# Kernel tuning notes

Hardware: AMD Instinct MI355X
Metric: run time of the kernel (lower is better)

Reference implementation:

```python
import jax, jax.numpy as jnp
import numpy as np

B, S, D, H = 4, 2048, 1024, 16
DH = D // H  # dim per head

def setup_inputs() -> dict:
    key = jax.random.key(0)
    ks = jax.random.split(key, 12)
    sc = 1.0 / np.sqrt(D)
    inp = {
        "key": jax.random.normal(ks[0], (B, S, D), jnp.float32),
        "value": jax.random.normal(ks[1], (B, S, D), jnp.float32),
        "query": jax.random.normal(ks[2], (B, S, D), jnp.float32),
        "mask": jax.random.randint(ks[3], (B, S, S), 0, 2).astype(bool),
        "Wq": jax.random.normal(ks[4], (D, D), jnp.float32) * sc,
        "bq": jnp.zeros((D,), jnp.float32),
        "Wk": jax.random.normal(ks[5], (D, D), jnp.float32) * sc,
        "bk": jnp.zeros((D,), jnp.float32),
        "Wv": jax.random.normal(ks[6], (D, D), jnp.float32) * sc,
        "bv": jnp.zeros((D,), jnp.float32),
        "Wo": jax.random.normal(ks[7], (D, D), jnp.float32) * sc,
        "bo": jnp.zeros((D,), jnp.float32),
    }
    return inp

def _shape(x, b):
    # [b, len, D] -> [b, H, len, DH]
    return x.reshape(b, -1, H, DH).transpose(0, 2, 1, 3)

def reference(key, value, query, mask, Wq, bq, Wk, bk, Wv, bv, Wo, bo):
    b = key.shape[0]
    q = _shape(query @ Wq.T + bq, b) / jnp.sqrt(jnp.asarray(DH, query.dtype))
    k = _shape(key @ Wk.T + bk, b)
    v = _shape(value @ Wv.T + bv, b)
    # scores: [b, H, q_len, k_len]
    scores = jnp.einsum("bhqd,bhkd->bhqk", q, k)
    scores = jnp.where(mask[:, None, :, :], jnp.asarray(-1e18, scores.dtype), scores)
    attn = jax.nn.softmax(scores, axis=-1)  # dropout is identity in eval mode
    ctx = jnp.einsum("bhqk,bhkd->bhqd", attn, v)
    ctx = ctx.transpose(0, 2, 1, 3).reshape(b, -1, H * DH)
    return ctx @ Wo.T + bo
```

## Files before the change

kernel.cpp:

```cpp
#include <hip/hip_runtime.h>

#define BB  4
#define SS  2048
#define DD  1024
#define HH  16
#define DHH 64
#define LOG2E 1.44269504088896340736f

typedef __attribute__((ext_vector_type(8)))  _Float16 half8;
typedef __attribute__((ext_vector_type(4)))  _Float16 half4;
typedef __attribute__((ext_vector_type(2)))  float    f32x2;
typedef __attribute__((ext_vector_type(4)))  float    f32x4;
typedef __attribute__((ext_vector_type(8)))  float    f32x8;
typedef __attribute__((ext_vector_type(16))) float    f32x16;
typedef __attribute__((ext_vector_type(4)))  unsigned int uint4v;

#if __has_builtin(__builtin_amdgcn_exp2f)
#define EXP2(x) __builtin_amdgcn_exp2f(x)
#else
#define EXP2(x) exp2f(x)
#endif

#if __has_builtin(__builtin_amdgcn_sbfe)
#define SBIT(x, p) __builtin_amdgcn_sbfe((int)(x), (unsigned)(p), 1u)
#else
#define SBIT(x, p) (((int)((x) << (31 - (p)))) >> 31)
#endif

__device__ __forceinline__ void gload_lds16(const void* g, void* l) {
  __builtin_amdgcn_global_load_lds(
      (const __attribute__((address_space(1))) unsigned int*)g,
      (__attribute__((address_space(3))) unsigned int*)l, 16, 0, 0);
}

__device__ __forceinline__ void plswap(unsigned int& x, unsigned int& y) {
  auto r = __builtin_amdgcn_permlane32_swap(x, y, false, false);
  x = r[0]; y = r[1];
}
__device__ __forceinline__ float xhalf_sum(float v) {
  unsigned int x = __builtin_bit_cast(unsigned int, v), y = x;
  plswap(x, y);
  return __builtin_bit_cast(float, x) + __builtin_bit_cast(float, y);
}

__device__ __forceinline__ float tree8(f32x8 u) {
  f32x4 v = __builtin_shufflevector(u, u, 0, 1, 2, 3) +
            __builtin_shufflevector(u, u, 4, 5, 6, 7);
  f32x2 w2 = __builtin_shufflevector(v, v, 0, 1) + __builtin_shufflevector(v, v, 2, 3);
  return w2[0] + w2[1];
}

__global__ __launch_bounds__(256) void cvt_f32_f16(
    const float* __restrict__ in, _Float16* __restrict__ out, int n4) {
  int i = blockIdx.x * 256 + threadIdx.x;
  if (i >= n4) return;
  float4 a = reinterpret_cast<const float4*>(in)[i];
  half4 h;
  h[0] = (_Float16)a.x; h[1] = (_Float16)a.y;
  h[2] = (_Float16)a.z; h[3] = (_Float16)a.w;
  reinterpret_cast<half4*>(out)[i] = h;
}

__global__ __launch_bounds__(256) void cvt_in3(
    const float* __restrict__ s0, const float* __restrict__ s1,
    const float* __restrict__ s2,
    _Float16* __restrict__ d0, _Float16* __restrict__ d1,
    _Float16* __restrict__ d2, int n4) {
  int i = blockIdx.x * 256 + threadIdx.x;
  if (i >= n4) return;
  const float* s; _Float16* d;
  switch (blockIdx.y) {
    case 0: s = s0; d = d0; break;
    case 1: s = s1; d = d1; break;
    default: s = s2; d = d2; break;
  }
  float4 a = reinterpret_cast<const float4*>(s)[i];
  half4 h;
  h[0] = (_Float16)a.x; h[1] = (_Float16)a.y;
  h[2] = (_Float16)a.z; h[3] = (_Float16)a.w;
  reinterpret_cast<half4*>(d)[i] = h;
}

__global__ __launch_bounds__(256) void cvt_w4(
    const float* __restrict__ s0, const float* __restrict__ s1,
    const float* __restrict__ s2, const float* __restrict__ s3,
    _Float16* __restrict__ d0, _Float16* __restrict__ d1,
    _Float16* __restrict__ d2, _Float16* __restrict__ d3, int n4) {
  int i = blockIdx.x * 256 + threadIdx.x;
  if (i >= n4) return;
  const float* s; _Float16* d;
  switch (blockIdx.y) {
    case 0: s = s0; d = d0; break;
    case 1: s = s1; d = d1; break;
    case 2: s = s2; d = d2; break;
    default: s = s3; d = d3; break;
  }
  float4 a = reinterpret_cast<const float4*>(s)[i];
  half4 h;
  h[0] = (_Float16)a.x; h[1] = (_Float16)a.y;
  h[2] = (_Float16)a.z; h[3] = (_Float16)a.w;
  reinterpret_cast<half4*>(d)[i] = h;
}

__global__ __launch_bounds__(256) void pack_mask_kernel(
    const int* __restrict__ m, unsigned long long* __restrict__ bitsT) {
  size_t g = (size_t)blockIdx.x * 256 + threadIdx.x;
  unsigned long long bal = __ballot(m[g] != 0);
  if ((threadIdx.x & 63) == 0) {
    int key = (int)(g & (SS - 1));
    int q   = (int)((g >> 11) & (SS - 1));
    int b   = (int)(g >> 22);
    bitsT[((size_t)(b * (SS / 64) + (key >> 6))) * SS + q] = bal;
  }
}


#define GEMM_BODY(A, Bm, K)                                                       \
  __shared__ _Float16 lsA[128 * 64];                                              \
  __shared__ _Float16 lsB[128 * 64];                                              \
  const int t = threadIdx.x;                                                      \
  const int w = t >> 6, l = t & 63;                                               \
  const int l15 = l & 15, l4 = l >> 4;                                            \
  const int wm = (w >> 1) * 64, wn = (w & 1) * 64;                                \
  const int srow = l >> 3;                                                        \
  const int scolh = ((l & 7) ^ srow) * 8;                                         \
  f32x4 acc[4][4] = {};                                                           \
  const _Float16* gA = (A) + (size_t)(tm * 128) * (K);                            \
  const _Float16* gB = (Bm) + (size_t)(tn * 128) * (K);                           \
  for (int kt = 0; kt < (K); kt += 64) {                                          \
    _Pragma("unroll") for (int i = 0; i < 4; ++i) {                               \
      int c = w * 4 + i;                                                          \
      int row = c * 8 + srow;                                                     \
      gload_lds16(gA + (size_t)row * (K) + kt + scolh, lsA + c * 512);            \
      gload_lds16(gB + (size_t)row * (K) + kt + scolh, lsB + c * 512);            \
    }                                                                             \
    __syncthreads();                                                              \
    _Pragma("unroll") for (int kk = 0; kk < 2; ++kk) {                            \
      half8 aF[4], bF[4];                                                         \
      _Pragma("unroll") for (int x = 0; x < 4; ++x) {                             \
        int ra = wm + x * 16 + l15;                                               \
        aF[x] = *(const half8*)(lsA + ra * 64 + ((kk * 32 + l4 * 8) ^ ((ra & 7) * 8))); \
        int rb = wn + x * 16 + l15;                                               \
        bF[x] = *(const half8*)(lsB + rb * 64 + ((kk * 32 + l4 * 8) ^ ((rb & 7) * 8))); \
      }                                                                           \
      _Pragma("unroll") for (int x = 0; x < 4; ++x)                               \
        _Pragma("unroll") for (int y = 0; y < 4; ++y)                             \
          acc[x][y] = __builtin_amdgcn_mfma_f32_16x16x32_f16(aF[x], bF[y], acc[x][y], 0, 0, 0); \
    }                                                                             \
    __syncthreads();                                                              \
  }

template <int MODE>
__global__ __launch_bounds__(256, 3) void gemm_nt(
    const _Float16* __restrict__ A, const _Float16* __restrict__ Bm,
    const float* __restrict__ bias, void* __restrict__ out,
    int M, int N, int K, int tilesN) {
  const int nb8 = gridDim.x >> 3;
  const int bidx = (blockIdx.x & 7) * nb8 + (blockIdx.x >> 3);
  const int tm = bidx / tilesN, tn = bidx % tilesN;
  GEMM_BODY(A, Bm, K)
#pragma unroll
  for (int x = 0; x < 4; ++x) {
#pragma unroll
    for (int r = 0; r < 4; ++r) {
      int i = tm * 128 + wm + x * 16 + l4 * 4 + r;
#pragma unroll
      for (int y = 0; y < 4; ++y) {
        int j = tn * 128 + wn + y * 16 + l15;
        float v = acc[x][y][r];
        if (MODE == 0) {
          v = (v + bias[j]) * (0.125f * LOG2E);
          ((_Float16*)out)[(((size_t)(i >> 11) * HH + (j >> 6)) * SS + (i & (SS - 1))) * DHH + (j & 63)] =
              (_Float16)v;
        } else if (MODE == 1) {
          v = v + bias[j];
          ((_Float16*)out)[(((size_t)(i >> 11) * HH + (j >> 6)) * SS + (i & (SS - 1))) * DHH + (j & 63)] =
              (_Float16)v;
        } else if (MODE == 2) {
          v = v + bias[i];
          ((_Float16*)out)[((size_t)(j >> 11) * DD + i) * SS + (j & (SS - 1))] = (_Float16)v;
        } else {
          ((float*)out)[(size_t)i * N + j] = v + bias[j];
        }
      }
    }
  }
}

__global__ __launch_bounds__(256, 3) void gemm_qk(
    const _Float16* __restrict__ xq, const _Float16* __restrict__ xk,
    const _Float16* __restrict__ wq, const _Float16* __restrict__ wk,
    const float* __restrict__ bq, const float* __restrict__ bk,
    _Float16* __restrict__ qh, _Float16* __restrict__ kh) {
  const int bidx = (blockIdx.x & 7) * 128 + (blockIdx.x >> 3);
  const int half = bidx >> 9;
  const int hb = bidx & 511;
  const int tm = hb >> 3, tn = hb & 7;
  const _Float16* A  = half ? xk : xq;
  const _Float16* Bm = half ? wk : wq;
  const float* bias  = half ? bk : bq;
  _Float16* dst      = half ? kh : qh;
  const float scl    = half ? 1.0f : (0.125f * LOG2E);
  GEMM_BODY(A, Bm, DD)
#pragma unroll
  for (int x = 0; x < 4; ++x) {
#pragma unroll
    for (int r = 0; r < 4; ++r) {
      int i = tm * 128 + wm + x * 16 + l4 * 4 + r;
#pragma unroll
      for (int y = 0; y < 4; ++y) {
        int j = tn * 128 + wn + y * 16 + l15;
        float v = (acc[x][y][r] + bias[j]) * scl;
        dst[(((size_t)(i >> 11) * HH + (j >> 6)) * SS + (i & (SS - 1))) * DHH + (j & 63)] =
            (_Float16)v;
      }
    }
  }
}

__global__ __launch_bounds__(256, 4) void attn_kernel(
    const _Float16* __restrict__ qh, const _Float16* __restrict__ kh,
    const _Float16* __restrict__ vt, const unsigned long long* __restrict__ mT,
    _Float16* __restrict__ ctx) {
  __shared__ _Float16 lsK[2][64 * 64];
  __shared__ _Float16 lsV[2][64 * 64];

  const int t = threadIdx.x;
  const int w = t >> 6, l = t & 63;
  const int l31 = l & 31, hi = l >> 5;
  const int srow = l >> 3;
  const int scolh = ((l & 7) ^ srow) * 8;

  const int bid = ((blockIdx.x & 7) << 7) | (blockIdx.x >> 3);
  const int bh = bid >> 4;
  const int qt = bid & 15;
  const int b = bh >> 4;
  const int h = bh & 15;
  const int qbase = qt * 128 + w * 32;

  const _Float16* qrow = qh + ((size_t)bh * SS + qbase + l31) * DHH + hi * 8;
  half8 bQ[4];
#pragma unroll
  for (int s = 0; s < 4; ++s) bQ[s] = *(const half8*)(qrow + s * 16);

  const _Float16* kbh = kh + (size_t)bh * SS * DHH;
  const _Float16* vbh = vt + (size_t)bh * DHH * SS;

  int boff[2][4];
  {
    const int swzb = (l31 & 7) * 16;
#pragma unroll
    for (int i = 0; i < 2; ++i)
#pragma unroll
      for (int s = 0; s < 4; ++s)
        boff[i][s] = (i * 32 + l31) * 128 + (((s * 16 + hi * 8) * 2) ^ swzb);
  }

  int ko0 = (w * 16 + srow) * DHH + scolh;
  int ko1 = ko0 + 8 * DHH;
  int vo0 = (w * 16 + srow) * SS + scolh;
  int vo1 = vo0 + 8 * SS;
  char* lsKb = (char*)&lsK[0][0];
  char* lsVb = (char*)&lsV[0][0];
  const int ldsb = w * 2048;

  f32x16 o0 = {}, o1 = {};
  f32x8 lsum8 = {};

  const unsigned long long* mp = mT + (size_t)b * (SS / 64) * SS + qbase + l31;
  unsigned long long mb = mp[0];

  gload_lds16(kbh + ko0, lsKb + ldsb);
  gload_lds16(kbh + ko1, lsKb + ldsb + 1024);
  gload_lds16(vbh + vo0, lsVb + ldsb);
  gload_lds16(vbh + vo1, lsVb + ldsb + 1024);
  ko0 += 64 * DHH; ko1 += 64 * DHH; vo0 += 64; vo1 += 64;

#pragma unroll 1
  for (int kt = 0; kt < 32; ++kt) {
    const int curb = (kt & 1) << 13;
    const int othb = curb ^ 8192;
    __syncthreads();
    if (kt < 31) {
      gload_lds16(kbh + ko0, lsKb + othb + ldsb);
      gload_lds16(kbh + ko1, lsKb + othb + ldsb + 1024);
      gload_lds16(vbh + vo0, lsVb + othb + ldsb);
      gload_lds16(vbh + vo1, lsVb + othb + ldsb + 1024);
      ko0 += 64 * DHH; ko1 += 64 * DHH; vo0 += 64; vo1 += 64;
    }
    unsigned long long mbn = 0;
    if (kt < 31) mbn = mp[(size_t)(kt + 1) * SS];

    const unsigned int mw0 = ((unsigned int)mb) >> (hi * 4);
    const unsigned int mw1 = ((unsigned int)(mb >> 32)) >> (hi * 4);
    const char* kbase = lsKb + curb;
    const char* vbase = lsVb + curb;

#pragma unroll
    for (int ns = 0; ns < 2; ++ns) {
      const unsigned int mwx = ns ? mw1 : mw0;
      f32x16 sc;
#pragma unroll
      for (int r = 0; r < 16; ++r) {
        const int p = (r & 3) + 8 * (r >> 2);
        sc[r] = __builtin_bit_cast(float,
            ((unsigned int)SBIT(mwx, p)) & 0xFF800000u);
      }
      __builtin_amdgcn_s_setprio(1);
#pragma unroll
      for (int s = 0; s < 4; ++s) {
        half8 aK = *(const half8*)(kbase + boff[ns][s]);
        sc = __builtin_amdgcn_mfma_f32_32x32x16_f16(aK, bQ[s], sc, 0, 0, 0);
      }
      __builtin_amdgcn_s_setprio(0);
#pragma unroll
      for (int hf = 0; hf < 2; ++hf) {
        const int e = hf * 8;
        float e0 = EXP2(sc[e + 0]);
        float e1 = EXP2(sc[e + 1]);
        float e2 = EXP2(sc[e + 2]);
        float e3 = EXP2(sc[e + 3]);
        float e4 = EXP2(sc[e + 4]);
        float e5 = EXP2(sc[e + 5]);
        float e6 = EXP2(sc[e + 6]);
        float e7 = EXP2(sc[e + 7]);
        lsum8[0] += e0; lsum8[1] += e1; lsum8[2] += e2; lsum8[3] += e3;
        lsum8[4] += e4; lsum8[5] += e5; lsum8[6] += e6; lsum8[7] += e7;
        unsigned int pa = __builtin_bit_cast(unsigned int,
            __builtin_amdgcn_cvt_pkrtz(e0, e1));
        unsigned int pb = __builtin_bit_cast(unsigned int,
            __builtin_amdgcn_cvt_pkrtz(e2, e3));
        unsigned int pc = __builtin_bit_cast(unsigned int,
            __builtin_amdgcn_cvt_pkrtz(e4, e5));
        unsigned int pd = __builtin_bit_cast(unsigned int,
            __builtin_amdgcn_cvt_pkrtz(e6, e7));
        plswap(pa, pc);
        plswap(pb, pd);
        uint4v u4 = {pa, pb, pc, pd};
        half8 aP = __builtin_bit_cast(half8, u4);
        const int s = ns * 2 + hf;
        half8 bV0 = *(const half8*)(vbase + boff[0][s]);
        half8 bV1 = *(const half8*)(vbase + boff[1][s]);
        __builtin_amdgcn_s_setprio(1);
        o0 = __builtin_amdgcn_mfma_f32_32x32x16_f16(aP, bV0, o0, 0, 0, 0);
        o1 = __builtin_amdgcn_mfma_f32_32x32x16_f16(aP, bV1, o1, 0, 0, 0);
        __builtin_amdgcn_s_setprio(0);
      }
    }
    mb = mbn;
  }

  const float lrun = xhalf_sum(tree8(lsum8));
  const float inv = 1.0f / lrun;
  _Float16* cbase = ctx + ((size_t)b * SS + qbase) * DD + h * DHH + l31;
#pragma unroll
  for (int r = 0; r < 16; ++r) {
    const int qr = (r & 3) + 8 * (r >> 2) + hi * 4;
    float ir = __shfl(inv, qr);
    cbase[(size_t)qr * DD]      = (_Float16)(o0[r] * ir);
    cbase[(size_t)qr * DD + 32] = (_Float16)(o1[r] * ir);
  }
}

extern "C" void kernel_launch(void* const* d_in, const int* in_sizes, int n_in,
                              void* d_out, int out_size, void* d_ws, size_t ws_size,
                              hipStream_t stream) {
  const float* key   = (const float*)d_in[0];
  const float* value = (const float*)d_in[1];
  const float* query = (const float*)d_in[2];
  const int*   mask  = (const int*)d_in[3];
  const float* Wq = (const float*)d_in[4];
  const float* bq = (const float*)d_in[5];
  const float* Wk = (const float*)d_in[6];
  const float* bk = (const float*)d_in[7];
  const float* Wv = (const float*)d_in[8];
  const float* bv = (const float*)d_in[9];
  const float* Wo = (const float*)d_in[10];
  const float* bo = (const float*)d_in[11];
  float* out = (float*)d_out;

  char* ws = (char*)d_ws;
  const int n4_in = BB * SS * DD / 4;
  const int n4_w  = DD * DD / 4;
  const size_t MB = 1048576;

  if (ws_size >= 106 * MB) {
    _Float16* xq = (_Float16*)(ws);
    _Float16* xk = (_Float16*)(ws + 16 * MB);
    _Float16* xv = (_Float16*)(ws + 32 * MB);
    _Float16* wq16 = (_Float16*)(ws + 48 * MB);
    _Float16* wk16 = (_Float16*)(ws + 50 * MB);
    _Float16* wv16 = (_Float16*)(ws + 52 * MB);
    _Float16* wo16 = (_Float16*)(ws + 54 * MB);
    _Float16* qh = (_Float16*)(ws + 56 * MB);
    _Float16* kh = (_Float16*)(ws + 72 * MB);
    _Float16* vt = (_Float16*)(ws + 88 * MB);
    unsigned long long* mbitsT = (unsigned long long*)(ws + 104 * MB);
    _Float16* ctx = xq;

    pack_mask_kernel<<<BB * SS * SS / 64 / 4, 256, 0, stream>>>(mask, mbitsT);
    cvt_w4<<<dim3(n4_w / 256, 4), 256, 0, stream>>>(Wq, Wk, Wv, Wo, wq16, wk16, wv16, wo16, n4_w);
    cvt_in3<<<dim3(n4_in / 256, 3), 256, 0, stream>>>(query, key, value, xq, xk, xv, n4_in);
    gemm_qk<<<1024, 256, 0, stream>>>(xq, xk, wq16, wk16, bq, bk, qh, kh);
    gemm_nt<2><<<512, 256, 0, stream>>>(wv16, xv, bv, vt, DD, BB * SS, DD, BB * SS / 128);
    attn_kernel<<<BB * HH * (SS / 128), 256, 0, stream>>>(qh, kh, vt, mbitsT, ctx);
    gemm_nt<3><<<512, 256, 0, stream>>>(ctx, wo16, bo, out, BB * SS, DD, DD, DD / 128);
  } else {
    _Float16* x16  = (_Float16*)(ws);
    _Float16* wq16 = (_Float16*)(ws + 16777216);
    _Float16* wk16 = (_Float16*)(ws + 18874368);
    _Float16* wv16 = (_Float16*)(ws + 20971520);
    _Float16* wo16 = (_Float16*)(ws + 23068672);
    _Float16* qh   = (_Float16*)(ws + 25165824);
    _Float16* kh   = (_Float16*)(ws + 41943040);
    _Float16* vt   = (_Float16*)(ws + 58720256);
    unsigned long long* mbitsT = (unsigned long long*)(ws + 75497472);
    _Float16* ctx = x16;

    pack_mask_kernel<<<BB * SS * SS / 64 / 4, 256, 0, stream>>>(mask, mbitsT);
    cvt_w4<<<dim3(n4_w / 256, 4), 256, 0, stream>>>(Wq, Wk, Wv, Wo, wq16, wk16, wv16, wo16, n4_w);
    cvt_f32_f16<<<n4_in / 256, 256, 0, stream>>>(query, x16, n4_in);
    gemm_nt<0><<<512, 256, 0, stream>>>(x16, wq16, bq, qh, BB * SS, DD, DD, DD / 128);
    cvt_f32_f16<<<n4_in / 256, 256, 0, stream>>>(key, x16, n4_in);
    gemm_nt<1><<<512, 256, 0, stream>>>(x16, wk16, bk, kh, BB * SS, DD, DD, DD / 128);
    cvt_f32_f16<<<n4_in / 256, 256, 0, stream>>>(value, x16, n4_in);
    gemm_nt<2><<<512, 256, 0, stream>>>(wv16, x16, bv, vt, DD, BB * SS, DD, BB * SS / 128);
    attn_kernel<<<BB * HH * (SS / 128), 256, 0, stream>>>(qh, kh, vt, mbitsT, ctx);
    gemm_nt<3><<<512, 256, 0, stream>>>(ctx, wo16, bo, out, BB * SS, DD, DD, DD / 128);
  }
}
```

Before: 258.3 us.

## Fuse fp32-to-fp16 input conversion into QKV projection GEMM loads

Drops the separate cvt_in3 pass over query/key/value. The Q/K and V projection GEMMs now read fp32 activations directly, convert them to fp16 in registers and store them to LDS. This saves writing and rereading 48MB of fp16 intermediates. In exchange the GEMM loads become synchronous register round-trips instead of direct global-to-LDS loads, and each activation tile is read as fp32 by every N-tile block, so the GEMMs read more global memory and may expose more load latency.

```diff
diff --git a/kernel.cpp b/kernel.cpp
--- a/kernel.cpp
+++ b/kernel.cpp
@@ -31,6 +31,17 @@
   __builtin_amdgcn_global_load_lds(
       (const __attribute__((address_space(1))) unsigned int*)g,
       (__attribute__((address_space(3))) unsigned int*)l, 16, 0, 0);
+}
+
+__device__ __forceinline__ void stage_cvt8(const float* g, _Float16* lds_chunk, int l) {
+  float4 a = *(const float4*)g;
+  float4 b = *(const float4*)(g + 4);
+  half8 h;
+  h[0] = (_Float16)a.x; h[1] = (_Float16)a.y;
+  h[2] = (_Float16)a.z; h[3] = (_Float16)a.w;
+  h[4] = (_Float16)b.x; h[5] = (_Float16)b.y;
+  h[6] = (_Float16)b.z; h[7] = (_Float16)b.w;
+  *(half8*)(lds_chunk + l * 8) = h;
 }
 
 __device__ __forceinline__ void plswap(unsigned int& x, unsigned int& y) {
@@ -59,26 +70,6 @@
   h[0] = (_Float16)a.x; h[1] = (_Float16)a.y;
   h[2] = (_Float16)a.z; h[3] = (_Float16)a.w;
   reinterpret_cast<half4*>(out)[i] = h;
-}
-
-__global__ __launch_bounds__(256) void cvt_in3(
-    const float* __restrict__ s0, const float* __restrict__ s1,
-    const float* __restrict__ s2,
-    _Float16* __restrict__ d0, _Float16* __restrict__ d1,
-    _Float16* __restrict__ d2, int n4) {
-  int i = blockIdx.x * 256 + threadIdx.x;
-  if (i >= n4) return;
-  const float* s; _Float16* d;
-  switch (blockIdx.y) {
-    case 0: s = s0; d = d0; break;
-    case 1: s = s1; d = d1; break;
-    default: s = s2; d = d2; break;
-  }
-  float4 a = reinterpret_cast<const float4*>(s)[i];
-  half4 h;
-  h[0] = (_Float16)a.x; h[1] = (_Float16)a.y;
-  h[2] = (_Float16)a.z; h[3] = (_Float16)a.w;
-  reinterpret_cast<half4*>(d)[i] = h;
 }
 
 __global__ __launch_bounds__(256) void cvt_w4(
@@ -114,51 +105,73 @@
   }
 }
 
-
-#define GEMM_BODY(A, Bm, K)                                                       \
-  __shared__ _Float16 lsA[128 * 64];                                              \
-  __shared__ _Float16 lsB[128 * 64];                                              \
-  const int t = threadIdx.x;                                                      \
-  const int w = t >> 6, l = t & 63;                                               \
-  const int l15 = l & 15, l4 = l >> 4;                                            \
-  const int wm = (w >> 1) * 64, wn = (w & 1) * 64;                                \
-  const int srow = l >> 3;                                                        \
-  const int scolh = ((l & 7) ^ srow) * 8;                                         \
-  f32x4 acc[4][4] = {};                                                           \
-  const _Float16* gA = (A) + (size_t)(tm * 128) * (K);                            \
-  const _Float16* gB = (Bm) + (size_t)(tn * 128) * (K);                           \
-  for (int kt = 0; kt < (K); kt += 64) {                                          \
-    _Pragma("unroll") for (int i = 0; i < 4; ++i) {                               \
-      int c = w * 4 + i;                                                          \
-      int row = c * 8 + srow;                                                     \
-      gload_lds16(gA + (size_t)row * (K) + kt + scolh, lsA + c * 512);            \
-      gload_lds16(gB + (size_t)row * (K) + kt + scolh, lsB + c * 512);            \
-    }                                                                             \
-    __syncthreads();                                                              \
-    _Pragma("unroll") for (int kk = 0; kk < 2; ++kk) {                            \
-      half8 aF[4], bF[4];                                                         \
-      _Pragma("unroll") for (int x = 0; x < 4; ++x) {                             \
-        int ra = wm + x * 16 + l15;                                               \
-        aF[x] = *(const half8*)(lsA + ra * 64 + ((kk * 32 + l4 * 8) ^ ((ra & 7) * 8))); \
-        int rb = wn + x * 16 + l15;                                               \
-        bF[x] = *(const half8*)(lsB + rb * 64 + ((kk * 32 + l4 * 8) ^ ((rb & 7) * 8))); \
-      }                                                                           \
-      _Pragma("unroll") for (int x = 0; x < 4; ++x)                               \
-        _Pragma("unroll") for (int y = 0; y < 4; ++y)                             \
-          acc[x][y] = __builtin_amdgcn_mfma_f32_16x16x32_f16(aF[x], bF[y], acc[x][y], 0, 0, 0); \
-    }                                                                             \
-    __syncthreads();                                                              \
-  }
+template <bool CVTA, bool CVTB>
+__device__ __forceinline__ void gemm_core(
+    const void* __restrict__ Ablk, const void* __restrict__ Bblk, int K,
+    int w, int l, _Float16* lsA, _Float16* lsB, f32x4 (&acc)[4][4]) {
+  const int l15 = l & 15, l4 = l >> 4;
+  const int wm = (w >> 1) * 64, wn = (w & 1) * 64;
+  const int srow = l >> 3;
+  const int scolh = ((l & 7) ^ srow) * 8;
+
+  for (int kt = 0; kt < K; kt += 64) {
+#pragma unroll
+    for (int i = 0; i < 4; ++i) {
+      int c = w * 4 + i;
+      int row = c * 8 + srow;
+      if constexpr (CVTA) {
+        stage_cvt8((const float*)Ablk + (size_t)row * K + kt + scolh,
+                   lsA + c * 512, l);
+      } else {
+        gload_lds16((const _Float16*)Ablk + (size_t)row * K + kt + scolh,
+                    lsA + c * 512);
+      }
+      if constexpr (CVTB) {
+        stage_cvt8((const float*)Bblk + (size_t)row * K + kt + scolh,
+                   lsB + c * 512, l);
+      } else {
+        gload_lds16((const _Float16*)Bblk + (size_t)row * K + kt + scolh,
+                    lsB + c * 512);
+      }
+    }
+    __syncthreads();
+#pragma unroll
+    for (int kk = 0; kk < 2; ++kk) {
+      half8 aF[4], bF[4];
+#pragma unroll
+      for (int x = 0; x < 4; ++x) {
+        int ra = wm + x * 16 + l15;
+        aF[x] = *(const half8*)(lsA + ra * 64 + ((kk * 32 + l4 * 8) ^ ((ra & 7) * 8)));
+        int rb = wn + x * 16 + l15;
+        bF[x] = *(const half8*)(lsB + rb * 64 + ((kk * 32 + l4 * 8) ^ ((rb & 7) * 8)));
+      }
+#pragma unroll
+      for (int x = 0; x < 4; ++x)
+#pragma unroll
+        for (int y = 0; y < 4; ++y)
+          acc[x][y] = __builtin_amdgcn_mfma_f32_16x16x32_f16(aF[x], bF[y], acc[x][y], 0, 0, 0);
+    }
+    __syncthreads();
+  }
+}
 
 template <int MODE>
 __global__ __launch_bounds__(256, 3) void gemm_nt(
     const _Float16* __restrict__ A, const _Float16* __restrict__ Bm,
     const float* __restrict__ bias, void* __restrict__ out,
     int M, int N, int K, int tilesN) {
+  __shared__ _Float16 lsA[128 * 64];
+  __shared__ _Float16 lsB[128 * 64];
+  const int t = threadIdx.x, w = t >> 6, l = t & 63;
   const int nb8 = gridDim.x >> 3;
   const int bidx = (blockIdx.x & 7) * nb8 + (blockIdx.x >> 3);
   const int tm = bidx / tilesN, tn = bidx % tilesN;
-  GEMM_BODY(A, Bm, K)
+  f32x4 acc[4][4] = {};
+  gemm_core<false, false>((const void*)(A + (size_t)(tm * 128) * K),
+                          (const void*)(Bm + (size_t)(tn * 128) * K),
+                          K, w, l, lsA, lsB, acc);
+  const int l15 = l & 15, l4 = l >> 4;
+  const int wm = (w >> 1) * 64, wn = (w & 1) * 64;
 #pragma unroll
   for (int x = 0; x < 4; ++x) {
 #pragma unroll
@@ -188,20 +201,28 @@
 }
 
 __global__ __launch_bounds__(256, 3) void gemm_qk(
-    const _Float16* __restrict__ xq, const _Float16* __restrict__ xk,
+    const float* __restrict__ q32, const float* __restrict__ k32,
     const _Float16* __restrict__ wq, const _Float16* __restrict__ wk,
     const float* __restrict__ bq, const float* __restrict__ bk,
     _Float16* __restrict__ qh, _Float16* __restrict__ kh) {
+  __shared__ _Float16 lsA[128 * 64];
+  __shared__ _Float16 lsB[128 * 64];
+  const int t = threadIdx.x, w = t >> 6, l = t & 63;
   const int bidx = (blockIdx.x & 7) * 128 + (blockIdx.x >> 3);
   const int half = bidx >> 9;
   const int hb = bidx & 511;
   const int tm = hb >> 3, tn = hb & 7;
-  const _Float16* A  = half ? xk : xq;
+  const float* A     = half ? k32 : q32;
   const _Float16* Bm = half ? wk : wq;
   const float* bias  = half ? bk : bq;
   _Float16* dst      = half ? kh : qh;
   const float scl    = half ? 1.0f : (0.125f * LOG2E);
-  GEMM_BODY(A, Bm, DD)
+  f32x4 acc[4][4] = {};
+  gemm_core<true, false>((const void*)(A + (size_t)(tm * 128) * DD),
+                         (const void*)(Bm + (size_t)(tn * 128) * DD),
+                         DD, w, l, lsA, lsB, acc);
+  const int l15 = l & 15, l4 = l >> 4;
+  const int wm = (w >> 1) * 64, wn = (w & 1) * 64;
 #pragma unroll
   for (int x = 0; x < 4; ++x) {
 #pragma unroll
@@ -213,6 +234,35 @@
         float v = (acc[x][y][r] + bias[j]) * scl;
         dst[(((size_t)(i >> 11) * HH + (j >> 6)) * SS + (i & (SS - 1))) * DHH + (j & 63)] =
             (_Float16)v;
+      }
+    }
+  }
+}
+
+__global__ __launch_bounds__(256, 3) void gemm_v(
+    const _Float16* __restrict__ wv, const float* __restrict__ v32,
+    const float* __restrict__ bv, _Float16* __restrict__ vt) {
+  __shared__ _Float16 lsA[128 * 64];
+  __shared__ _Float16 lsB[128 * 64];
+  const int t = threadIdx.x, w = t >> 6, l = t & 63;
+  const int bidx = (blockIdx.x & 7) * 64 + (blockIdx.x >> 3);
+  const int tm = bidx >> 6, tn = bidx & 63;
+  f32x4 acc[4][4] = {};
+  gemm_core<false, true>((const void*)(wv + (size_t)(tm * 128) * DD),
+                         (const void*)(v32 + (size_t)(tn * 128) * DD),
+                         DD, w, l, lsA, lsB, acc);
+  const int l15 = l & 15, l4 = l >> 4;
+  const int wm = (w >> 1) * 64, wn = (w & 1) * 64;
+#pragma unroll
+  for (int x = 0; x < 4; ++x) {
+#pragma unroll
+    for (int r = 0; r < 4; ++r) {
+      int i = tm * 128 + wm + x * 16 + l4 * 4 + r;
+#pragma unroll
+      for (int y = 0; y < 4; ++y) {
+        int j = tn * 128 + wn + y * 16 + l15;
+        float v = acc[x][y][r] + bv[i];
+        vt[((size_t)(j >> 11) * DD + i) * SS + (j & (SS - 1))] = (_Float16)v;
       }
     }
   }
@@ -384,25 +434,21 @@
   const int n4_w  = DD * DD / 4;
   const size_t MB = 1048576;
 
-  if (ws_size >= 106 * MB) {
-    _Float16* xq = (_Float16*)(ws);
-    _Float16* xk = (_Float16*)(ws + 16 * MB);
-    _Float16* xv = (_Float16*)(ws + 32 * MB);
-    _Float16* wq16 = (_Float16*)(ws + 48 * MB);
-    _Float16* wk16 = (_Float16*)(ws + 50 * MB);
-    _Float16* wv16 = (_Float16*)(ws + 52 * MB);
-    _Float16* wo16 = (_Float16*)(ws + 54 * MB);
-    _Float16* qh = (_Float16*)(ws + 56 * MB);
-    _Float16* kh = (_Float16*)(ws + 72 * MB);
-    _Float16* vt = (_Float16*)(ws + 88 * MB);
-    unsigned long long* mbitsT = (unsigned long long*)(ws + 104 * MB);
-    _Float16* ctx = xq;
+  if (ws_size >= 80 * MB) {
+    _Float16* wq16 = (_Float16*)(ws);
+    _Float16* wk16 = (_Float16*)(ws + 2 * MB);
+    _Float16* wv16 = (_Float16*)(ws + 4 * MB);
+    _Float16* wo16 = (_Float16*)(ws + 6 * MB);
+    _Float16* qh   = (_Float16*)(ws + 8 * MB);
+    _Float16* kh   = (_Float16*)(ws + 24 * MB);
+    _Float16* vt   = (_Float16*)(ws + 40 * MB);
+    _Float16* ctx  = (_Float16*)(ws + 56 * MB);
+    unsigned long long* mbitsT = (unsigned long long*)(ws + 72 * MB);
 
     pack_mask_kernel<<<BB * SS * SS / 64 / 4, 256, 0, stream>>>(mask, mbitsT);
     cvt_w4<<<dim3(n4_w / 256, 4), 256, 0, stream>>>(Wq, Wk, Wv, Wo, wq16, wk16, wv16, wo16, n4_w);
-    cvt_in3<<<dim3(n4_in / 256, 3), 256, 0, stream>>>(query, key, value, xq, xk, xv, n4_in);
-    gemm_qk<<<1024, 256, 0, stream>>>(xq, xk, wq16, wk16, bq, bk, qh, kh);
-    gemm_nt<2><<<512, 256, 0, stream>>>(wv16, xv, bv, vt, DD, BB * SS, DD, BB * SS / 128);
+    gemm_qk<<<1024, 256, 0, stream>>>(query, key, wq16, wk16, bq, bk, qh, kh);
+    gemm_v<<<512, 256, 0, stream>>>(wv16, value, bv, vt);
     attn_kernel<<<BB * HH * (SS / 128), 256, 0, stream>>>(qh, kh, vt, mbitsT, ctx);
     gemm_nt<3><<<512, 256, 0, stream>>>(ctx, wo16, bo, out, BB * SS, DD, DD, DD / 128);
   } else {
```

Result: slower. 336.0 us (+30.1%).
